# Kernel tuning notes

Hardware: AMD Instinct MI355X
Metric: run time of the kernel (lower is better)

## Reference

```python
import jax, jax.numpy as jnp
import numpy as np

ANNOT = 512
HID = 64
N_STEPS = 8
N_NODES = 100000
N_EDGES = 1600000
NUM_GRAPHS = 64


def setup_inputs() -> dict:
    key = jax.random.key(0)
    ks = jax.random.split(key, 16)
    s = 0.05
    x = jax.random.normal(ks[0], (N_NODES, ANNOT), dtype=jnp.float32)
    edge_index = jax.random.randint(ks[1], (2, N_EDGES), 0, N_NODES, dtype=jnp.int64)
    batch = jnp.sort(jax.random.randint(ks[2], (N_NODES,), 0, NUM_GRAPHS, dtype=jnp.int64))
    return {
        "x": x,
        "edge_index": edge_index,
        "batch": batch,
        "reduce_w": jax.random.normal(ks[3], (ANNOT, HID), dtype=jnp.float32) * s,
        "reduce_b": jnp.zeros((HID,), dtype=jnp.float32),
        "ggc_weight": jax.random.normal(ks[4], (N_STEPS, HID, HID), dtype=jnp.float32) * s,
        "gru_w_ih": jax.random.normal(ks[5], (3 * HID, HID), dtype=jnp.float32) * s,
        "gru_w_hh": jax.random.normal(ks[6], (3 * HID, HID), dtype=jnp.float32) * s,
        "gru_b_ih": jnp.zeros((3 * HID,), dtype=jnp.float32),
        "gru_b_hh": jnp.zeros((3 * HID,), dtype=jnp.float32),
        "gate_w": jax.random.normal(ks[7], (HID, 1), dtype=jnp.float32) * s,
        "gate_b": jnp.zeros((1,), dtype=jnp.float32),
        "out_w": jax.random.normal(ks[8], (HID, 2), dtype=jnp.float32) * s,
        "out_b": jnp.zeros((2,), dtype=jnp.float32),
    }


def _gru_cell(m, h, w_ih, w_hh, b_ih, b_hh):
    gi = m @ w_ih.T + b_ih  # [N, 3H]
    gh = h @ w_hh.T + b_hh
    i_r, i_z, i_n = jnp.split(gi, 3, axis=-1)
    h_r, h_z, h_n = jnp.split(gh, 3, axis=-1)
    r = jax.nn.sigmoid(i_r + h_r)
    z = jax.nn.sigmoid(i_z + h_z)
    n = jnp.tanh(i_n + r * h_n)
    return (1.0 - z) * n + z * h


def _segment_softmax(logits, seg, num_segments):
    # logits: [N, 1]; per-graph softmax (PyG softmax with 1e-16 eps)
    m = jax.ops.segment_max(logits, seg, num_segments=num_segments)
    e = jnp.exp(logits - m[seg])
    s = jax.ops.segment_sum(e, seg, num_segments=num_segments)
    return e / (s[seg] + 1e-16)


def reference(x, edge_index, batch, reduce_w, reduce_b, ggc_weight,
              gru_w_ih, gru_w_hh, gru_b_ih, gru_b_hh,
              gate_w, gate_b, out_w, out_b):
    n_nodes = x.shape[0]
    src, dst = edge_index[0], edge_index[1]

    # reduce: annotation -> hidden
    h = x @ reduce_w + reduce_b  # [N, H]

    # GatedGraphConv: n_steps of (linear -> gather -> scatter-add -> GRU)
    def step(h, W):
        m = h @ W  # [N, H]
        aggr = jax.ops.segment_sum(m[src], dst, num_segments=n_nodes)  # scatter-add
        h_new = _gru_cell(aggr, h, gru_w_ih, gru_w_hh, gru_b_ih, gru_b_hh)
        return h_new, None

    h, _ = jax.lax.scan(step, h, ggc_weight)

    # GlobalAttention pooling: gate_nn -> per-graph softmax; nn -> features
    gate = _segment_softmax(h @ gate_w + gate_b, batch, NUM_GRAPHS)  # [N, 1]
    feat = h @ out_w + out_b  # [N, 2]
    pooled = jax.ops.segment_sum(gate * feat, batch, num_segments=NUM_GRAPHS)  # [G, 2]

    return jax.nn.softmax(pooled, axis=1)
```

## Files before the change

### kernel.cpp

```cpp
#include <hip/hip_runtime.h>
#include <math.h>

#define HID 64
#define ANNOT 512
#define NSTEPS 8
#define PCHUNK 4096
#define CSR_CAP 10240

typedef __attribute__((ext_vector_type(8))) short short8_t;
typedef __attribute__((ext_vector_type(16))) float floatx16;

__device__ __forceinline__ float sigmoidf_(float x) { return 1.0f / (1.0f + __expf(-x)); }

__device__ __forceinline__ float bf2f(unsigned short u) {
  return __uint_as_float(((unsigned)u) << 16);
}
__device__ __forceinline__ unsigned short f2bf(float f) {
  unsigned u = __float_as_uint(f);
  unsigned r = ((u >> 16) & 1u) + 0x7fffu;
  return (unsigned short)((u + r) >> 16);
}
__device__ __forceinline__ float bflo(unsigned u) { return __uint_as_float(u << 16); }
__device__ __forceinline__ float bfhi(unsigned u) { return __uint_as_float(u & 0xffff0000u); }
__device__ __forceinline__ unsigned cvtpk_bf16(float lo, float hi) {
  unsigned r;
  asm("v_cvt_pk_bf16_f32 %0, %1, %2" : "=v"(r) : "v"(lo), "v"(hi));
  return r;
}

__global__ void k_wpack(const float* __restrict__ Wr, unsigned short* __restrict__ Wpack) {
  const int t = blockIdx.x;
  const int kc = t >> 1, nt = t & 1;
  const int l = threadIdx.x;
  const int c = nt * 32 + (l & 31);
  unsigned short* dst = Wpack + ((size_t)t * 64 + l) * 8;
#pragma unroll
  for (int j = 0; j < 8; ++j) {
    int k = kc * 16 + (l >> 5) * 8 + j;
    dst[j] = f2bf(Wr[(size_t)k * HID + c]);
  }
}

__global__ __launch_bounds__(256) void k_reduce(
    const float* __restrict__ x, const unsigned short* __restrict__ Wpack,
    const float* __restrict__ br, unsigned short* __restrict__ h, int n_nodes)
{
  const int wave = threadIdx.x >> 6;
  const int lane = threadIdx.x & 63;
  const int hi = lane >> 5;
  const int l31 = lane & 31;
  const int rbase = blockIdx.x * 128 + wave * 32;
  const int arow = rbase + l31;
  const bool avalid = arow < n_nodes;
  const float* xrow = x + (size_t)arow * ANNOT + hi * 8;

  floatx16 acc[2];
#pragma unroll
  for (int nt = 0; nt < 2; ++nt)
#pragma unroll
    for (int j = 0; j < 16; ++j) acc[nt][j] = 0.f;

#pragma unroll 4
  for (int kc = 0; kc < 32; ++kc) {
    short8_t a = {0, 0, 0, 0, 0, 0, 0, 0};
    if (avalid) {
      float4 u0 = *(const float4*)(xrow + kc * 16);
      float4 u1 = *(const float4*)(xrow + kc * 16 + 4);
      int4 ai;
      ai.x = (int)cvtpk_bf16(u0.x, u0.y);
      ai.y = (int)cvtpk_bf16(u0.z, u0.w);
      ai.z = (int)cvtpk_bf16(u1.x, u1.y);
      ai.w = (int)cvtpk_bf16(u1.z, u1.w);
      a = *(short8_t*)&ai;
    }
    const short8_t* Bb = (const short8_t*)(Wpack + (size_t)kc * 2 * 64 * 8);
#pragma unroll
    for (int nt = 0; nt < 2; ++nt) {
      short8_t b = Bb[nt * 64 + lane];
      acc[nt] = __builtin_amdgcn_mfma_f32_32x32x16_bf16(a, b, acc[nt], 0, 0, 0);
    }
  }

  float bias[2];
  bias[0] = br[l31];
  bias[1] = br[32 + l31];
#pragma unroll
  for (int reg = 0; reg < 16; ++reg) {
    int row = rbase + (reg & 3) + 8 * (reg >> 2) + 4 * hi;
    if (row < n_nodes) {
#pragma unroll
      for (int nt = 0; nt < 2; ++nt) {
        float v = acc[nt][reg] + bias[nt];
        h[(size_t)row * HID + nt * 32 + l31] = f2bf(v);
      }
    }
  }
}

__global__ void k_bbig(const float* __restrict__ ggc_w, const float* __restrict__ w_ih,
                       const float* __restrict__ w_hh, unsigned short* __restrict__ Bpack)
{
  const int nt = blockIdx.x;
  const int kc = blockIdx.y;
  const int s  = blockIdx.z;
  const int l  = threadIdx.x;
  const int c = nt * 32 + (l & 31);
  const int sec = c >> 6, f = c & 63;
  unsigned short outv[8];
#pragma unroll
  for (int j = 0; j < 8; ++j) {
    int k = kc * 16 + (l >> 5) * 8 + j;
    float v = 0.f;
    if (k < 64) {
      if (sec < 3) {
        const float* Ws = ggc_w + ((size_t)s * 64 + k) * 64;
        const float* wr = w_ih + (size_t)(sec * 64 + f) * 64;
        float a = 0.f;
        for (int q = 0; q < 64; ++q) a += Ws[q] * wr[q];
        v = a;
      }
    } else {
      int k2 = k - 64;
      if (sec == 0)      v = w_hh[(size_t)f * 64 + k2];
      else if (sec == 1) v = w_hh[(size_t)(64 + f) * 64 + k2];
      else if (sec == 3) v = w_hh[(size_t)(128 + f) * 64 + k2];
    }
    outv[j] = f2bf(v);
  }
  unsigned short* dst = Bpack + ((((size_t)s * 8 + kc) * 8 + nt) * 64 + l) * 8;
#pragma unroll
  for (int j = 0; j < 8; ++j) dst[j] = outv[j];
}

__global__ __launch_bounds__(256) void k_pcnt(const int* __restrict__ dstv, int E,
                                              int* __restrict__ bukCnt, int nbuk)
{
  __shared__ int lh[256];
  lh[threadIdx.x] = 0;
  __syncthreads();
  for (int e = blockIdx.x * blockDim.x + threadIdx.x; e < E; e += gridDim.x * blockDim.x)
    atomicAdd(&lh[dstv[e] >> 9], 1);
  __syncthreads();
  if (threadIdx.x < nbuk) {
    int v = lh[threadIdx.x];
    if (v) atomicAdd(&bukCnt[threadIdx.x], v);
  }
}

__global__ void k_bscan(const int* __restrict__ bukCnt, int nbuk,
                        int* __restrict__ bukBase, int* __restrict__ bukCur,
                        int* __restrict__ row_ptr, int n_nodes, int E)
{
  if (threadIdx.x == 0 && blockIdx.x == 0) {
    int run = 0;
    for (int b = 0; b < nbuk; ++b) { bukBase[b] = run; bukCur[b] = run; run += bukCnt[b]; }
    bukBase[nbuk] = run;
    row_ptr[n_nodes] = E;
  }
}

__global__ __launch_bounds__(256) void k_part(
    const int* __restrict__ srcv, const int* __restrict__ dstv, int E,
    int* __restrict__ bukCur, unsigned* __restrict__ rec, int nbuk)
{
  __shared__ int lhist[256], lexcl[256], lbase[256], lcur[256];
  __shared__ unsigned lrec[PCHUNK];
  __shared__ unsigned char lbuk[PCHUNK];
  const int t = threadIdx.x;
  const int nchunk = (E + PCHUNK - 1) / PCHUNK;
  for (int c = blockIdx.x; c < nchunk; c += gridDim.x) {
    const int e0 = c * PCHUNK;
    const int cnt = min(PCHUNK, E - e0);
    lhist[t] = 0;
    __syncthreads();
    int myS[16], myD[16];
#pragma unroll
    for (int i = 0; i < 16; ++i) {
      int j = t + i * 256;
      myS[i] = -1; myD[i] = 0;
      if (j < cnt) {
        int e = e0 + j;
        myS[i] = srcv[e];
        myD[i] = dstv[e];
        atomicAdd(&lhist[myD[i] >> 9], 1);
      }
    }
    __syncthreads();
    int v = lhist[t];
    lexcl[t] = v;
    __syncthreads();
    for (int d = 1; d < 256; d <<= 1) {
      int u = (t >= d) ? lexcl[t - d] : 0;
      __syncthreads();
      lexcl[t] += u;
      __syncthreads();
    }
    int excl = lexcl[t] - v;
    __syncthreads();
    lexcl[t] = excl;
    lcur[t] = excl;
    if (v > 0) lbase[t] = atomicAdd(&bukCur[t], v);
    __syncthreads();
#pragma unroll
    for (int i = 0; i < 16; ++i) {
      if (myS[i] >= 0) {
        int b = myD[i] >> 9;
        int p = atomicAdd(&lcur[b], 1);
        lrec[p] = (unsigned)myS[i] | ((unsigned)(myD[i] & 511) << 23);
        lbuk[p] = (unsigned char)b;
      }
    }
    __syncthreads();
    for (int j = t; j < cnt; j += 256) {
      int b = lbuk[j];
      rec[(size_t)lbase[b] + (j - lexcl[b])] = lrec[j];
    }
    __syncthreads();
  }
}

__global__ __launch_bounds__(512) void k_csr(
    const unsigned* __restrict__ rec, const int* __restrict__ bukBase,
    int* __restrict__ row_ptr, int* __restrict__ csr_src, int n_nodes)
{
  __shared__ int cnt[512], off[512], cur[512];
  __shared__ int outbuf[CSR_CAP];
  const int b = blockIdx.x;
  const int t = threadIdx.x;
  const int beg = bukBase[b], end = bukBase[b + 1];
  const int m = end - beg;
  const int node0 = b << 9;
  cnt[t] = 0;
  __syncthreads();
  for (int j = t; j < m; j += 512)
    atomicAdd(&cnt[rec[beg + j] >> 23], 1);
  __syncthreads();
  int v = cnt[t];
  off[t] = v;
  __syncthreads();
  for (int d = 1; d < 512; d <<= 1) {
    int u = (t >= d) ? off[t - d] : 0;
    __syncthreads();
    off[t] += u;
    __syncthreads();
  }
  int excl = off[t] - v;
  cur[t] = excl;
  int node = node0 + t;
  if (node < n_nodes) row_ptr[node] = beg + excl;
  __syncthreads();
  for (int j = t; j < m; j += 512) {
    unsigned r = rec[beg + j];
    int p = atomicAdd(&cur[r >> 23], 1);
    if (p < CSR_CAP) outbuf[p] = (int)(r & 0x7FFFFFu);
  }
  __syncthreads();
  for (int j = t; j < m; j += 512)
    csr_src[beg + j] = (j < CSR_CAP) ? outbuf[j] : 0;
}

__global__ __launch_bounds__(256) void k_aggr(
    const uint4* __restrict__ h16, const int* __restrict__ row_ptr,
    const int* __restrict__ csr_src, uint4* __restrict__ aggr16, int n_nodes)
{
  const int wid = threadIdx.x >> 6;
  const int lane = threadIdx.x & 63;
  const int grp = lane >> 3;
  const int l8 = lane & 7;
  const int n = blockIdx.x * 4 + wid;
  if (n >= n_nodes) return;
  const int beg = row_ptr[n], end = row_ptr[n + 1];
  const int last = end - 1;
  float a0 = 0.f, a1 = 0.f, a2 = 0.f, a3 = 0.f, a4 = 0.f, a5 = 0.f, a6 = 0.f, a7 = 0.f;

  for (int eb = beg; eb < end; eb += 32) {
    const int e0 = eb + grp * 4;
    int s0 = csr_src[min(e0,     last)]; if (e0     > last) s0 = n_nodes;
    int s1 = csr_src[min(e0 + 1, last)]; if (e0 + 1 > last) s1 = n_nodes;
    int s2 = csr_src[min(e0 + 2, last)]; if (e0 + 2 > last) s2 = n_nodes;
    int s3 = csr_src[min(e0 + 3, last)]; if (e0 + 3 > last) s3 = n_nodes;
    uint4 v0 = h16[(size_t)s0 * 8 + l8];
    uint4 v1 = h16[(size_t)s1 * 8 + l8];
    uint4 v2 = h16[(size_t)s2 * 8 + l8];
    uint4 v3 = h16[(size_t)s3 * 8 + l8];
    a0 += bflo(v0.x) + bflo(v1.x) + bflo(v2.x) + bflo(v3.x);
    a1 += bfhi(v0.x) + bfhi(v1.x) + bfhi(v2.x) + bfhi(v3.x);
    a2 += bflo(v0.y) + bflo(v1.y) + bflo(v2.y) + bflo(v3.y);
    a3 += bfhi(v0.y) + bfhi(v1.y) + bfhi(v2.y) + bfhi(v3.y);
    a4 += bflo(v0.z) + bflo(v1.z) + bflo(v2.z) + bflo(v3.z);
    a5 += bfhi(v0.z) + bfhi(v1.z) + bfhi(v2.z) + bfhi(v3.z);
    a6 += bflo(v0.w) + bflo(v1.w) + bflo(v2.w) + bflo(v3.w);
    a7 += bfhi(v0.w) + bfhi(v1.w) + bfhi(v2.w) + bfhi(v3.w);
  }

#pragma unroll
  for (int d = 8; d <= 32; d <<= 1) {
    a0 += __shfl_xor(a0, d); a1 += __shfl_xor(a1, d);
    a2 += __shfl_xor(a2, d); a3 += __shfl_xor(a3, d);
    a4 += __shfl_xor(a4, d); a5 += __shfl_xor(a5, d);
    a6 += __shfl_xor(a6, d); a7 += __shfl_xor(a7, d);
  }

  if (lane < 8) {
    uint4 o;
    o.x = cvtpk_bf16(a0, a1);
    o.y = cvtpk_bf16(a2, a3);
    o.z = cvtpk_bf16(a4, a5);
    o.w = cvtpk_bf16(a6, a7);
    aggr16[(size_t)n * 8 + lane] = o;
  }
}

__global__ __launch_bounds__(256) void k_gru(
    const unsigned short* __restrict__ aggr, unsigned short* __restrict__ h,
    const unsigned short* __restrict__ Bpack_s,
    const float* __restrict__ b_ih, const float* __restrict__ b_hh, int n_nodes)
{
  const int wave = threadIdx.x >> 6;
  const int lane = threadIdx.x & 63;
  const int hi = lane >> 5;
  const int l31 = lane & 31;
  const int rbase = blockIdx.x * 128 + wave * 32;
  const int arow = rbase + l31;
  const bool avalid = arow < n_nodes;

  floatx16 acc[8];
#pragma unroll
  for (int nt = 0; nt < 8; ++nt)
#pragma unroll
    for (int j = 0; j < 16; ++j) acc[nt][j] = 0.f;

#pragma unroll
  for (int kc = 0; kc < 8; ++kc) {
    const unsigned short* Asrc = (kc < 4) ? aggr : h;
    short8_t a = {0, 0, 0, 0, 0, 0, 0, 0};
    if (avalid)
      a = *(const short8_t*)(Asrc + (size_t)arow * HID + (kc & 3) * 16 + hi * 8);
    const short8_t* Bb = (const short8_t*)(Bpack_s + (size_t)kc * 8 * 64 * 8);
#pragma unroll
    for (int nt = 0; nt < 8; ++nt) {
      short8_t b = Bb[nt * 64 + lane];
      acc[nt] = __builtin_amdgcn_mfma_f32_32x32x16_bf16(a, b, acc[nt], 0, 0, 0);
    }
  }

  float bi[2][3], bh[2][3];
#pragma unroll
  for (int half = 0; half < 2; ++half) {
    int f = half * 32 + l31;
    bi[half][0] = b_ih[f]; bi[half][1] = b_ih[64 + f]; bi[half][2] = b_ih[128 + f];
    bh[half][0] = b_hh[f]; bh[half][1] = b_hh[64 + f]; bh[half][2] = b_hh[128 + f];
  }
#pragma unroll
  for (int reg = 0; reg < 16; ++reg) {
    int row = rbase + (reg & 3) + 8 * (reg >> 2) + 4 * hi;
    if (row < n_nodes) {
#pragma unroll
      for (int half = 0; half < 2; ++half) {
        int f = half * 32 + l31;
        float rg = sigmoidf_(acc[half][reg] + bi[half][0] + bh[half][0]);
        float zg = sigmoidf_(acc[2 + half][reg] + bi[half][1] + bh[half][1]);
        float ng = tanhf(acc[4 + half][reg] + bi[half][2] + rg * (acc[6 + half][reg] + bh[half][2]));
        size_t idx = (size_t)row * HID + f;
        float hold = bf2f(h[idx]);
        h[idx] = f2bf((1.f - zg) * ng + zg * hold);
      }
    }
  }
}

__global__ __launch_bounds__(256) void k_pool(
    const unsigned short* __restrict__ h, const int* __restrict__ batch,
    const float* __restrict__ gate_w, const float* __restrict__ gate_b,
    const float* __restrict__ out_w, const float* __restrict__ out_b,
    float* __restrict__ acc3, int n_nodes)
{
  __shared__ float sacc[192];
  int t = threadIdx.x;
  if (t < 192) sacc[t] = 0.f;
  __syncthreads();
  int n = blockIdx.x * blockDim.x + t;
  if (n < n_nodes) {
    float g = gate_b[0], f0 = out_b[0], f1 = out_b[1];
    const ushort4* hr = (const ushort4*)(h + (size_t)n * HID);
#pragma unroll
    for (int q = 0; q < 16; ++q) {
      ushort4 v = hr[q];
      float h0 = bf2f(v.x), h1 = bf2f(v.y), h2 = bf2f(v.z), h3 = bf2f(v.w);
      int k = q * 4;
      g += h0 * gate_w[k] + h1 * gate_w[k + 1] + h2 * gate_w[k + 2] + h3 * gate_w[k + 3];
      f0 += h0 * out_w[2 * k] + h1 * out_w[2 * k + 2] + h2 * out_w[2 * k + 4] + h3 * out_w[2 * k + 6];
      f1 += h0 * out_w[2 * k + 1] + h1 * out_w[2 * k + 3] + h2 * out_w[2 * k + 5] + h3 * out_w[2 * k + 7];
    }
    float e = expf(g);
    int b = batch[n];
    atomicAdd(&sacc[3 * b + 0], e);
    atomicAdd(&sacc[3 * b + 1], e * f0);
    atomicAdd(&sacc[3 * b + 2], e * f1);
  }
  __syncthreads();
  if (t < 192) {
    float v = sacc[t];
    if (v != 0.f) atomicAdd(&acc3[t], v);
  }
}

__global__ void k_pool3(const float* __restrict__ acc3, float* __restrict__ out, int n_graphs) {
  int g = blockIdx.x * blockDim.x + threadIdx.x;
  if (g < n_graphs) {
    float s = acc3[3 * g] + 1e-16f;
    float p0 = acc3[3 * g + 1] / s, p1 = acc3[3 * g + 2] / s;
    float m = fmaxf(p0, p1);
    float e0 = expf(p0 - m), e1 = expf(p1 - m);
    float d = e0 + e1;
    out[2 * g] = e0 / d;
    out[2 * g + 1] = e1 / d;
  }
}

extern "C" void kernel_launch(void* const* d_in, const int* in_sizes, int n_in,
                              void* d_out, int out_size, void* d_ws, size_t ws_size,
                              hipStream_t stream)
{
  const float* x        = (const float*)d_in[0];
  const int*   edge     = (const int*)d_in[1];
  const int*   batch    = (const int*)d_in[2];
  const float* reduce_w = (const float*)d_in[3];
  const float* reduce_b = (const float*)d_in[4];
  const float* ggc_w    = (const float*)d_in[5];
  const float* w_ih     = (const float*)d_in[6];
  const float* w_hh     = (const float*)d_in[7];
  const float* b_ih     = (const float*)d_in[8];
  const float* b_hh     = (const float*)d_in[9];
  const float* gate_w   = (const float*)d_in[10];
  const float* gate_b   = (const float*)d_in[11];
  const float* out_w    = (const float*)d_in[12];
  const float* out_b    = (const float*)d_in[13];
  float* out = (float*)d_out;

  const int n_nodes  = in_sizes[0] / ANNOT;
  const int E        = in_sizes[1] / 2;
  const int n_graphs = out_size / 2;
  const int* src  = edge;
  const int* dstv = edge + E;
  const int nbuk = (n_nodes + 511) >> 9;

  size_t off = 0;
  auto alloc = [&](size_t bytes) { size_t o = off; off = (off + bytes + 255) & ~(size_t)255; return o; };
  char* w = (char*)d_ws;

  unsigned short* h    = (unsigned short*)(w + alloc((size_t)(n_nodes + 1) * HID * 2));
  unsigned short* aggr = (unsigned short*)(w + alloc((size_t)n_nodes * HID * 2));
  int*   csr_src = (int*)(w + alloc((size_t)E * 4));
  int*   row_ptr = (int*)(w + alloc((size_t)(n_nodes + 1) * 4));
  unsigned* rec  = (unsigned*)(w + alloc((size_t)E * 4));
  int*   bukCnt  = (int*)(w + alloc((size_t)(nbuk + 1) * 4));
  int*   bukBase = (int*)(w + alloc((size_t)(nbuk + 1) * 4));
  int*   bukCur  = (int*)(w + alloc((size_t)(nbuk + 1) * 4));
  unsigned short* Bpack = (unsigned short*)(w + alloc((size_t)NSTEPS * 8 * 8 * 64 * 8 * 2));
  unsigned short* Wpack = (unsigned short*)(w + alloc((size_t)64 * 64 * 8 * 2));
  float* acc3    = (float*)(w + alloc(192 * 4));
  (void)ws_size; (void)n_in;

  hipMemsetAsync(bukCnt, 0, (size_t)(nbuk + 1) * 4, stream);
  hipMemsetAsync(acc3, 0, 192 * 4, stream);
  hipMemsetAsync(h + (size_t)n_nodes * HID, 0, HID * 2, stream);

  const int gN256 = (n_nodes + 255) / 256;
  const int nchunk = (E + PCHUNK - 1) / PCHUNK;

  k_wpack<<<64, 64, 0, stream>>>(reduce_w, Wpack);
  k_reduce<<<(n_nodes + 127) / 128, 256, 0, stream>>>(x, Wpack, reduce_b, h, n_nodes);
  k_bbig<<<dim3(8, 8, NSTEPS), 64, 0, stream>>>(ggc_w, w_ih, w_hh, Bpack);

  k_pcnt<<<1024, 256, 0, stream>>>(dstv, E, bukCnt, nbuk);
  k_bscan<<<1, 1, 0, stream>>>(bukCnt, nbuk, bukBase, bukCur, row_ptr, n_nodes, E);
  k_part<<<nchunk, 256, 0, stream>>>(src, dstv, E, bukCur, rec, nbuk);
  k_csr<<<nbuk, 512, 0, stream>>>(rec, bukBase, row_ptr, csr_src, n_nodes);

  for (int s = 0; s < NSTEPS; ++s) {
    k_aggr<<<(n_nodes + 3) / 4, 256, 0, stream>>>((const uint4*)h, row_ptr, csr_src, (uint4*)aggr, n_nodes);
    k_gru<<<(n_nodes + 127) / 128, 256, 0, stream>>>(aggr, h, Bpack + (size_t)s * 8 * 8 * 64 * 8, b_ih, b_hh, n_nodes);
  }

  k_pool<<<gN256, 256, 0, stream>>>(h, batch, gate_w, gate_b, out_w, out_b, acc3, n_nodes);
  k_pool3<<<1, 64, 0, stream>>>(acc3, out, n_graphs);
}
```

Measured before the change: 682.6 us.

## Map one 8-lane group per node in aggregation instead of one wave

The aggregation kernel now gives each 8-lane group of a wave its own destination node, so a wave handles 8 nodes and a block handles 32. Each group walks its node's edges 4 at a time, and the cross-group shuffle reduction is removed. With an average in-degree of about 16, the old one-wave-per-node mapping left many lanes idle on padded edges. The new mapping risks divergence between groups whose nodes have unequal degrees, and each lane now issues more dependent loop iterations.

After: 652.9 us (median of 2 runs). -4.4%, faster.

```diff
diff --git a/kernel.cpp b/kernel.cpp
--- a/kernel.cpp
+++ b/kernel.cpp
@@ -267,18 +267,19 @@
   const int lane = threadIdx.x & 63;
   const int grp = lane >> 3;
   const int l8 = lane & 7;
-  const int n = blockIdx.x * 4 + wid;
-  if (n >= n_nodes) return;
-  const int beg = row_ptr[n], end = row_ptr[n + 1];
+  const int n = blockIdx.x * 32 + wid * 8 + grp;
+  const bool valid = n < n_nodes;
+  const int nc = valid ? n : (n_nodes - 1);
+  const int beg = row_ptr[nc];
+  const int end = valid ? row_ptr[nc + 1] : beg;
   const int last = end - 1;
   float a0 = 0.f, a1 = 0.f, a2 = 0.f, a3 = 0.f, a4 = 0.f, a5 = 0.f, a6 = 0.f, a7 = 0.f;
 
-  for (int eb = beg; eb < end; eb += 32) {
-    const int e0 = eb + grp * 4;
-    int s0 = csr_src[min(e0,     last)]; if (e0     > last) s0 = n_nodes;
-    int s1 = csr_src[min(e0 + 1, last)]; if (e0 + 1 > last) s1 = n_nodes;
-    int s2 = csr_src[min(e0 + 2, last)]; if (e0 + 2 > last) s2 = n_nodes;
-    int s3 = csr_src[min(e0 + 3, last)]; if (e0 + 3 > last) s3 = n_nodes;
+  for (int e = beg; e < end; e += 4) {
+    int s0 = csr_src[min(e,     last)]; if (e     > last) s0 = n_nodes;
+    int s1 = csr_src[min(e + 1, last)]; if (e + 1 > last) s1 = n_nodes;
+    int s2 = csr_src[min(e + 2, last)]; if (e + 2 > last) s2 = n_nodes;
+    int s3 = csr_src[min(e + 3, last)]; if (e + 3 > last) s3 = n_nodes;
     uint4 v0 = h16[(size_t)s0 * 8 + l8];
     uint4 v1 = h16[(size_t)s1 * 8 + l8];
     uint4 v2 = h16[(size_t)s2 * 8 + l8];
@@ -293,21 +294,13 @@
     a7 += bfhi(v0.w) + bfhi(v1.w) + bfhi(v2.w) + bfhi(v3.w);
   }
 
-#pragma unroll
-  for (int d = 8; d <= 32; d <<= 1) {
-    a0 += __shfl_xor(a0, d); a1 += __shfl_xor(a1, d);
-    a2 += __shfl_xor(a2, d); a3 += __shfl_xor(a3, d);
-    a4 += __shfl_xor(a4, d); a5 += __shfl_xor(a5, d);
-    a6 += __shfl_xor(a6, d); a7 += __shfl_xor(a7, d);
-  }
-
-  if (lane < 8) {
+  if (valid) {
     uint4 o;
     o.x = cvtpk_bf16(a0, a1);
     o.y = cvtpk_bf16(a2, a3);
     o.z = cvtpk_bf16(a4, a5);
     o.w = cvtpk_bf16(a6, a7);
-    aggr16[(size_t)n * 8 + lane] = o;
+    aggr16[(size_t)n * 8 + l8] = o;
   }
 }
 
@@ -479,7 +472,7 @@
   k_csr<<<nbuk, 512, 0, stream>>>(rec, bukBase, row_ptr, csr_src, n_nodes);
 
   for (int s = 0; s < NSTEPS; ++s) {
-    k_aggr<<<(n_nodes + 3) / 4, 256, 0, stream>>>((const uint4*)h, row_ptr, csr_src, (uint4*)aggr, n_nodes);
+    k_aggr<<<(n_nodes + 31) / 32, 256, 0, stream>>>((const uint4*)h, row_ptr, csr_src, (uint4*)aggr, n_nodes);
     k_gru<<<(n_nodes + 127) / 128, 256, 0, stream>>>(aggr, h, Bpack + (size_t)s * 8 * 8 * 64 * 8, b_ih, b_hh, n_nodes);
   }
 
```
